# Optimization experiments

Measured on AMD Instinct MI355X. Metric: run time of the kernel, lower is better.

## Reference

```python
import jax, jax.numpy as jnp
import numpy as np

SEQ_LEN, BATCH, INPUT_SIZE, HIDDEN_SIZE = 512, 256, 256, 1024
ALPHA = 10.0 / 100.0  # dt / tau


def setup_inputs() -> dict:
    key = jax.random.key(0)
    k1, k2, k3, k4, k5 = jax.random.split(key, 5)
    s_in = 1.0 / np.sqrt(INPUT_SIZE)
    s_hh = 1.0 / np.sqrt(HIDDEN_SIZE)
    return {
        "x": jax.random.normal(k1, (SEQ_LEN, BATCH, INPUT_SIZE), jnp.float32),
        "W_in": jax.random.uniform(k2, (HIDDEN_SIZE, INPUT_SIZE), jnp.float32, -s_in, s_in),
        "b_in": jax.random.uniform(k3, (HIDDEN_SIZE,), jnp.float32, -s_in, s_in),
        "W_hh": jax.random.uniform(k4, (HIDDEN_SIZE, HIDDEN_SIZE), jnp.float32, -s_hh, s_hh),
        "b_hh": jax.random.uniform(k5, (HIDDEN_SIZE,), jnp.float32, -s_hh, s_hh),
    }


def reference(x, W_in, b_in, W_hh, b_hh):
    # Precompute input projection for all steps as one batched GEMM: [T,B,H]
    inp_proj = jnp.einsum("tbi,hi->tbh", x, W_in) + b_in

    def step(hidden, u_t):
        h_new = jax.nn.relu(u_t + hidden @ W_hh.T + b_hh)
        h_new = hidden * (1.0 - ALPHA) + h_new * ALPHA
        return h_new, h_new

    h0 = jnp.zeros((x.shape[1], W_hh.shape[0]), x.dtype)
    hidden, output = jax.lax.scan(step, h0, inp_proj)
    return output, hidden
```

## Files before the change

kernel.cpp:

```cpp
#include <hip/hip_runtime.h>
#include <hip/hip_bf16.h>
#include <stdint.h>
#include <stddef.h>

#define T_LEN 512
#define B_SZ  256
#define I_SZ  256
#define H_SZ  1024
#define NGRP  16

typedef __attribute__((ext_vector_type(8))) short bf16x8;
typedef __attribute__((ext_vector_type(4))) float f32x4;
typedef __attribute__((ext_vector_type(4))) unsigned int u32x4;
typedef unsigned short u16;
typedef unsigned int   u32;
typedef unsigned long long u64;

__device__ inline u16 f2bf(float f) {
  union { float f; u32 u; } x; x.f = f;
  u32 r = x.u + 0x7fffu + ((x.u >> 16) & 1u);
  return (u16)(r >> 16);
}

#define GLDS16(gp, lp) __builtin_amdgcn_global_load_lds( \
    (const __attribute__((address_space(1))) u32*)(gp),  \
    (__attribute__((address_space(3))) u32*)(lp), 16, 0, 0)

#define PIN8(B, i) asm volatile("" : "+v"(B[i]), "+v"(B[i+1]), "+v"(B[i+2]), \
    "+v"(B[i+3]), "+v"(B[i+4]), "+v"(B[i+5]), "+v"(B[i+6]), "+v"(B[i+7]))
#define PIN32(B) do { PIN8(B,0); PIN8(B,8); PIN8(B,16); PIN8(B,24); } while (0)

struct GCnt { u32 v; u32 pad[31]; };

__global__ __launch_bounds__(256) void cvt_kernel(const float* __restrict__ src,
                                                  u16* __restrict__ dst, int n) {
  int stride = gridDim.x * blockDim.x * 4;
  for (int i = (blockIdx.x * blockDim.x + threadIdx.x) * 4; i < n; i += stride) {
    float4 v = *reinterpret_cast<const float4*>(src + i);
    ushort4 o;
    o.x = f2bf(v.x); o.y = f2bf(v.y); o.z = f2bf(v.z); o.w = f2bf(v.w);
    *reinterpret_cast<ushort4*>(dst + i) = o;
  }
}

__global__ __launch_bounds__(256) void stage1_gemm(const u16* __restrict__ A,
                                                   const u16* __restrict__ Bw,
                                                   const float* __restrict__ b_in,
                                                   float* __restrict__ C) {
  __shared__ __align__(16) u16 As[128 * 32];
  __shared__ __align__(16) u16 Bs[128 * 32];
  const int tid  = threadIdx.x;
  const int lane = tid & 63;
  const int wid  = tid >> 6;
  const int wr   = wid >> 1, wc = wid & 1;
  const int bm0  = blockIdx.x * 128;
  const int bn0  = blockIdx.y * 128;
  const int rl   = lane & 15;
  const int kl   = (lane >> 4) * 8;

  f32x4 acc[4][4];
  for (int mi = 0; mi < 4; ++mi)
    for (int ni = 0; ni < 4; ++ni)
      acc[mi][ni] = (f32x4){0.f, 0.f, 0.f, 0.f};

  for (int kt = 0; kt < I_SZ / 32; ++kt) {
    const int k0 = kt * 32;
    __syncthreads();
    for (int t2 = 0; t2 < 2; ++t2) {
      int c = t2 * 256 + tid;
      int row = c >> 2, c8 = c & 3;
      GLDS16(A  + (size_t)(bm0 + row) * I_SZ + k0 + c8 * 8, As + c * 8);
      GLDS16(Bw + (size_t)(bn0 + row) * I_SZ + k0 + c8 * 8, Bs + c * 8);
    }
    __syncthreads();
    bf16x8 af[4], bfv[4];
    for (int mi = 0; mi < 4; ++mi)
      af[mi] = *reinterpret_cast<const bf16x8*>(&As[(wr * 64 + mi * 16 + rl) * 32 + kl]);
    for (int ni = 0; ni < 4; ++ni)
      bfv[ni] = *reinterpret_cast<const bf16x8*>(&Bs[(wc * 64 + ni * 16 + rl) * 32 + kl]);
    for (int mi = 0; mi < 4; ++mi)
      for (int ni = 0; ni < 4; ++ni)
        acc[mi][ni] = __builtin_amdgcn_mfma_f32_16x16x32_bf16(af[mi], bfv[ni], acc[mi][ni], 0, 0, 0);
  }

  const int rh = (lane >> 4) * 4;
  for (int ni = 0; ni < 4; ++ni) {
    int col = bn0 + wc * 64 + ni * 16 + rl;
    float bi = b_in[col];
    for (int mi = 0; mi < 4; ++mi) {
      int row = bm0 + wr * 64 + mi * 16 + rh;
      f32x4 c = acc[mi][ni];
      for (int r = 0; r < 4; ++r)
        C[(size_t)(row + r) * H_SZ + col] = c[r] + bi;
    }
  }
}

__global__ __launch_bounds__(256, 1) void rnn_persistent(
    const u16* __restrict__ Whh, const float* __restrict__ b_hh,
    float* __restrict__ out, u16* __restrict__ hb0, u16* __restrict__ hb1,
    GCnt* __restrict__ cnts) {
  __shared__ __align__(16) u16 As[16 * 1024];

  const int b   = blockIdx.x;
  const int mg  = ((b & 7) << 1) | ((b >> 3) & 1);
  const int ng  = b >> 4;
  const int bm0 = mg * 16;
  const int bn0 = ng * 64;
  const int tid = threadIdx.x, lane = tid & 63, wid = tid >> 6;
  const int rl  = lane & 15, kq = lane >> 4;

  u32* cnt = &cnts[mg].v;

  const int wcol = bn0 + wid * 16 + rl;
  bf16x8 Breg[32];
#pragma unroll
  for (int kc = 0; kc < 32; ++kc)
    Breg[kc] = *reinterpret_cast<const bf16x8*>(Whh + (size_t)wcol * H_SZ + kc * 32 + kq * 8);
  PIN32(Breg);

  const int row = bm0 + rl;
  const int c0  = bn0 + wid * 16 + kq * 4;
  const float4 bh4 = *reinterpret_cast<const float4*>(b_hh + c0);

  float4 hprev = {0.f, 0.f, 0.f, 0.f};
  float4 u = *reinterpret_cast<const float4*>(out + (size_t)row * H_SZ + c0);
  const char* Asb = (const char*)As;

  const int wb = (tid & 127) * 16;
  const int rb = tid >> 7;

  for (int t = 0; t < T_LEN; ++t) {
    const u16* hin = (t & 1) ? hb1 : hb0;
    u16* hout      = (t & 1) ? hb0 : hb1;

    PIN32(Breg);

    u32x4 sv[8];
    const char* hinb = (const char*)hin;
#pragma unroll
    for (int i = 0; i < 8; ++i) {
      int r_ = 2 * i + rb;
      const void* src = hinb + (size_t)(bm0 + r_) * 2048 + wb;
      asm volatile("global_load_dwordx4 %0, %1, off sc0 sc1"
                   : "=v"(sv[i]) : "v"(src) : "memory");
    }
    asm volatile("s_waitcnt vmcnt(0)" ::: "memory");
    __builtin_amdgcn_sched_barrier(0);
#pragma unroll
    for (int i = 0; i < 8; ++i) {
      int r_ = 2 * i + rb;
      int dst = r_ * 2048 + (wb ^ ((r_ & 7) << 4));
      *reinterpret_cast<u32x4*>((char*)As + dst) = sv[i];
    }
    __syncthreads();

    float4 un = *reinterpret_cast<const float4*>(
        out + (size_t)(t + 1) * (B_SZ * H_SZ) + (size_t)row * H_SZ + c0);

    PIN32(Breg);

    f32x4 acc0 = (f32x4){0.f, 0.f, 0.f, 0.f};
    f32x4 acc1 = (f32x4){0.f, 0.f, 0.f, 0.f};
#pragma unroll
    for (int kc = 0; kc < 32; kc += 2) {
      bf16x8 a0 = *reinterpret_cast<const bf16x8*>(
          Asb + rl * 2048 + ((kc * 64 + kq * 16) ^ ((rl & 7) << 4)));
      acc0 = __builtin_amdgcn_mfma_f32_16x16x32_bf16(Breg[kc], a0, acc0, 0, 0, 0);
      bf16x8 a1 = *reinterpret_cast<const bf16x8*>(
          Asb + rl * 2048 + (((kc + 1) * 64 + kq * 16) ^ ((rl & 7) << 4)));
      acc1 = __builtin_amdgcn_mfma_f32_16x16x32_bf16(Breg[kc + 1], a1, acc1, 0, 0, 0);
    }

    float hv[4];
#pragma unroll
    for (int r = 0; r < 4; ++r) {
      float pre = (&u.x)[r] + acc0[r] + acc1[r] + (&bh4.x)[r];
      float hn  = fmaxf(pre, 0.f);
      float h   = (&hprev.x)[r] * 0.9f + hn * 0.1f;
      (&hprev.x)[r] = h;
      hv[r] = h;
    }
    u32 lo = (u32)f2bf(hv[0]) | ((u32)f2bf(hv[1]) << 16);
    u32 hi = (u32)f2bf(hv[2]) | ((u32)f2bf(hv[3]) << 16);
    u64 pk = (u64)lo | ((u64)hi << 32);
    __hip_atomic_store(reinterpret_cast<u64*>(hout + (size_t)row * H_SZ + c0), pk,
                       __ATOMIC_RELAXED, __HIP_MEMORY_SCOPE_AGENT);

    __syncthreads();
    if (t < T_LEN - 1 && tid == 0)
      __hip_atomic_fetch_add(cnt, 1u, __ATOMIC_RELAXED, __HIP_MEMORY_SCOPE_AGENT);

    float4 ho = {hv[0], hv[1], hv[2], hv[3]};
    *reinterpret_cast<float4*>(out + (size_t)t * (B_SZ * H_SZ) +
                               (size_t)row * H_SZ + c0) = ho;
    if (t == T_LEN - 1)
      *reinterpret_cast<float4*>(out + (size_t)T_LEN * (B_SZ * H_SZ) +
                                 (size_t)row * H_SZ + c0) = ho;
    u = un;

    if (t < T_LEN - 1) {
      if (tid == 0) {
        const u32 tgt = (u32)(NGRP * (t + 1));
        while (__hip_atomic_load(cnt, __ATOMIC_RELAXED, __HIP_MEMORY_SCOPE_AGENT) < tgt) {
        }
      }
      __syncthreads();
      __builtin_amdgcn_sched_barrier(0);
    }
  }
}

extern "C" void kernel_launch(void* const* d_in, const int* in_sizes, int n_in,
                              void* d_out, int out_size, void* d_ws, size_t ws_size,
                              hipStream_t stream) {
  const float* x    = (const float*)d_in[0];
  const float* W_in = (const float*)d_in[1];
  const float* b_in = (const float*)d_in[2];
  const float* W_hh = (const float*)d_in[3];
  const float* b_hh = (const float*)d_in[4];
  float* out = (float*)d_out;

  const size_t off_xb  = 0;
  const size_t off_wib = 67108864;
  const size_t off_whb = 67633152;
  const size_t off_hb0 = 69730304;
  const size_t off_hb1 = 70254592;
  const size_t need    = 70778880;
  if (ws_size < need) return;

  char* ws = (char*)d_ws;
  u16* xb   = (u16*)(ws + off_xb);
  u16* wib  = (u16*)(ws + off_wib);
  u16* whb  = (u16*)(ws + off_whb);
  u16* hb0  = (u16*)(ws + off_hb0);
  u16* hb1  = (u16*)(ws + off_hb1);
  GCnt* cnts = (GCnt*)(ws + 0);

  cvt_kernel<<<1024, 256, 0, stream>>>(x,    xb,  T_LEN * B_SZ * I_SZ);
  cvt_kernel<<<64,   256, 0, stream>>>(W_in, wib, H_SZ * I_SZ);
  cvt_kernel<<<256,  256, 0, stream>>>(W_hh, whb, H_SZ * H_SZ);
  hipMemsetAsync(hb0, 0, (size_t)B_SZ * H_SZ * sizeof(u16), stream);

  dim3 g1(T_LEN * B_SZ / 128, H_SZ / 128);
  stage1_gemm<<<g1, 256, 0, stream>>>(xb, wib, b_in, out);

  hipMemsetAsync(cnts, 0, NGRP * sizeof(GCnt), stream);

  rnn_persistent<<<256, 256, 0, stream>>>(whb, b_hh, out, hb0, hb1, cnts);
}
```

Measured before the change: 1.342 ms.

## Fuse input projection into persistent RNN kernel, drop stage1 GEMM

Removes the separate x conversion kernel and the stage-1 GEMM. W_in is now held in registers inside the persistent recurrent kernel, which converts the x slice for the next step to bf16 in LDS (double buffered) while waiting on the barrier, then adds it through extra MFMAs each step. This drops a large GEMM plus its write and read of the projection tensor. In exchange each step does more compute and global loads on the serial critical path, and register pressure rises.

```diff
diff --git a/kernel.cpp b/kernel.cpp
--- a/kernel.cpp
+++ b/kernel.cpp
@@ -21,10 +21,6 @@
   u32 r = x.u + 0x7fffu + ((x.u >> 16) & 1u);
   return (u16)(r >> 16);
 }
-
-#define GLDS16(gp, lp) __builtin_amdgcn_global_load_lds( \
-    (const __attribute__((address_space(1))) u32*)(gp),  \
-    (__attribute__((address_space(3))) u32*)(lp), 16, 0, 0)
 
 #define PIN8(B, i) asm volatile("" : "+v"(B[i]), "+v"(B[i+1]), "+v"(B[i+2]), \
     "+v"(B[i+3]), "+v"(B[i+4]), "+v"(B[i+5]), "+v"(B[i+6]), "+v"(B[i+7]))
@@ -43,64 +39,13 @@
   }
 }
 
-__global__ __launch_bounds__(256) void stage1_gemm(const u16* __restrict__ A,
-                                                   const u16* __restrict__ Bw,
-                                                   const float* __restrict__ b_in,
-                                                   float* __restrict__ C) {
-  __shared__ __align__(16) u16 As[128 * 32];
-  __shared__ __align__(16) u16 Bs[128 * 32];
-  const int tid  = threadIdx.x;
-  const int lane = tid & 63;
-  const int wid  = tid >> 6;
-  const int wr   = wid >> 1, wc = wid & 1;
-  const int bm0  = blockIdx.x * 128;
-  const int bn0  = blockIdx.y * 128;
-  const int rl   = lane & 15;
-  const int kl   = (lane >> 4) * 8;
-
-  f32x4 acc[4][4];
-  for (int mi = 0; mi < 4; ++mi)
-    for (int ni = 0; ni < 4; ++ni)
-      acc[mi][ni] = (f32x4){0.f, 0.f, 0.f, 0.f};
-
-  for (int kt = 0; kt < I_SZ / 32; ++kt) {
-    const int k0 = kt * 32;
-    __syncthreads();
-    for (int t2 = 0; t2 < 2; ++t2) {
-      int c = t2 * 256 + tid;
-      int row = c >> 2, c8 = c & 3;
-      GLDS16(A  + (size_t)(bm0 + row) * I_SZ + k0 + c8 * 8, As + c * 8);
-      GLDS16(Bw + (size_t)(bn0 + row) * I_SZ + k0 + c8 * 8, Bs + c * 8);
-    }
-    __syncthreads();
-    bf16x8 af[4], bfv[4];
-    for (int mi = 0; mi < 4; ++mi)
-      af[mi] = *reinterpret_cast<const bf16x8*>(&As[(wr * 64 + mi * 16 + rl) * 32 + kl]);
-    for (int ni = 0; ni < 4; ++ni)
-      bfv[ni] = *reinterpret_cast<const bf16x8*>(&Bs[(wc * 64 + ni * 16 + rl) * 32 + kl]);
-    for (int mi = 0; mi < 4; ++mi)
-      for (int ni = 0; ni < 4; ++ni)
-        acc[mi][ni] = __builtin_amdgcn_mfma_f32_16x16x32_bf16(af[mi], bfv[ni], acc[mi][ni], 0, 0, 0);
-  }
-
-  const int rh = (lane >> 4) * 4;
-  for (int ni = 0; ni < 4; ++ni) {
-    int col = bn0 + wc * 64 + ni * 16 + rl;
-    float bi = b_in[col];
-    for (int mi = 0; mi < 4; ++mi) {
-      int row = bm0 + wr * 64 + mi * 16 + rh;
-      f32x4 c = acc[mi][ni];
-      for (int r = 0; r < 4; ++r)
-        C[(size_t)(row + r) * H_SZ + col] = c[r] + bi;
-    }
-  }
-}
-
 __global__ __launch_bounds__(256, 1) void rnn_persistent(
-    const u16* __restrict__ Whh, const float* __restrict__ b_hh,
-    float* __restrict__ out, u16* __restrict__ hb0, u16* __restrict__ hb1,
-    GCnt* __restrict__ cnts) {
+    const float* __restrict__ x, const u16* __restrict__ Win,
+    const u16* __restrict__ Whh, const float* __restrict__ b_in,
+    const float* __restrict__ b_hh, float* __restrict__ out,
+    u16* __restrict__ hb0, u16* __restrict__ hb1, GCnt* __restrict__ cnts) {
   __shared__ __align__(16) u16 As[16 * 1024];
+  __shared__ __align__(16) u16 Xs[2][16 * 256];
 
   const int b   = blockIdx.x;
   const int mg  = ((b & 7) << 1) | ((b >> 3) & 1);
@@ -117,18 +62,50 @@
 #pragma unroll
   for (int kc = 0; kc < 32; ++kc)
     Breg[kc] = *reinterpret_cast<const bf16x8*>(Whh + (size_t)wcol * H_SZ + kc * 32 + kq * 8);
+  bf16x8 Wreg[8];
+#pragma unroll
+  for (int kc = 0; kc < 8; ++kc)
+    Wreg[kc] = *reinterpret_cast<const bf16x8*>(Win + (size_t)wcol * I_SZ + kc * 32 + kq * 8);
   PIN32(Breg);
+  PIN8(Wreg, 0);
 
   const int row = bm0 + rl;
   const int c0  = bn0 + wid * 16 + kq * 4;
-  const float4 bh4 = *reinterpret_cast<const float4*>(b_hh + c0);
+  float4 bsum;
+#pragma unroll
+  for (int r = 0; r < 4; ++r)
+    (&bsum.x)[r] = b_in[c0 + r] + b_hh[c0 + r];
 
   float4 hprev = {0.f, 0.f, 0.f, 0.f};
-  float4 u = *reinterpret_cast<const float4*>(out + (size_t)row * H_SZ + c0);
   const char* Asb = (const char*)As;
 
   const int wb = (tid & 127) * 16;
   const int rb = tid >> 7;
+
+  const int xc0 = tid * 2;
+
+  auto stage_x = [&](int s) {
+    const float* xs = x + (size_t)s * (B_SZ * I_SZ);
+#pragma unroll
+    for (int j = 0; j < 2; ++j) {
+      int c  = xc0 + j;
+      int r_ = c >> 5;
+      int cb = (c & 31) * 16;
+      const float* src = xs + (size_t)(bm0 + r_) * I_SZ + (c & 31) * 8;
+      float4 f0 = *reinterpret_cast<const float4*>(src);
+      float4 f1 = *reinterpret_cast<const float4*>(src + 4);
+      u32x4 v;
+      v.x = (u32)f2bf(f0.x) | ((u32)f2bf(f0.y) << 16);
+      v.y = (u32)f2bf(f0.z) | ((u32)f2bf(f0.w) << 16);
+      v.z = (u32)f2bf(f1.x) | ((u32)f2bf(f1.y) << 16);
+      v.w = (u32)f2bf(f1.z) | ((u32)f2bf(f1.w) << 16);
+      int dst = r_ * 512 + (cb ^ ((r_ & 7) << 4));
+      *reinterpret_cast<u32x4*>((char*)Xs[s & 1] + dst) = v;
+    }
+  };
+
+  stage_x(0);
+  __syncthreads();
 
   for (int t = 0; t < T_LEN; ++t) {
     const u16* hin = (t & 1) ? hb1 : hb0;
@@ -155,13 +132,11 @@
     }
     __syncthreads();
 
-    float4 un = *reinterpret_cast<const float4*>(
-        out + (size_t)(t + 1) * (B_SZ * H_SZ) + (size_t)row * H_SZ + c0);
-
     PIN32(Breg);
 
     f32x4 acc0 = (f32x4){0.f, 0.f, 0.f, 0.f};
     f32x4 acc1 = (f32x4){0.f, 0.f, 0.f, 0.f};
+    f32x4 acc2 = (f32x4){0.f, 0.f, 0.f, 0.f};
 #pragma unroll
     for (int kc = 0; kc < 32; kc += 2) {
       bf16x8 a0 = *reinterpret_cast<const bf16x8*>(
@@ -171,11 +146,20 @@
           Asb + rl * 2048 + (((kc + 1) * 64 + kq * 16) ^ ((rl & 7) << 4)));
       acc1 = __builtin_amdgcn_mfma_f32_16x16x32_bf16(Breg[kc + 1], a1, acc1, 0, 0, 0);
     }
+    {
+      const char* Xb = (const char*)Xs[t & 1];
+#pragma unroll
+      for (int kc = 0; kc < 8; ++kc) {
+        bf16x8 xa = *reinterpret_cast<const bf16x8*>(
+            Xb + rl * 512 + ((kc * 64 + kq * 16) ^ ((rl & 7) << 4)));
+        acc2 = __builtin_amdgcn_mfma_f32_16x16x32_bf16(Wreg[kc], xa, acc2, 0, 0, 0);
+      }
+    }
 
     float hv[4];
 #pragma unroll
     for (int r = 0; r < 4; ++r) {
-      float pre = (&u.x)[r] + acc0[r] + acc1[r] + (&bh4.x)[r];
+      float pre = acc0[r] + acc1[r] + acc2[r] + (&bsum.x)[r];
       float hn  = fmaxf(pre, 0.f);
       float h   = (&hprev.x)[r] * 0.9f + hn * 0.1f;
       (&hprev.x)[r] = h;
@@ -191,13 +175,13 @@
     if (t < T_LEN - 1 && tid == 0)
       __hip_atomic_fetch_add(cnt, 1u, __ATOMIC_RELAXED, __HIP_MEMORY_SCOPE_AGENT);
 
+    if (t < T_LEN - 1) stage_x(t + 1);
     float4 ho = {hv[0], hv[1], hv[2], hv[3]};
     *reinterpret_cast<float4*>(out + (size_t)t * (B_SZ * H_SZ) +
                                (size_t)row * H_SZ + c0) = ho;
     if (t == T_LEN - 1)
       *reinterpret_cast<float4*>(out + (size_t)T_LEN * (B_SZ * H_SZ) +
                                  (size_t)row * H_SZ + c0) = ho;
-    u = un;
 
     if (t < T_LEN - 1) {
       if (tid == 0) {
@@ -221,31 +205,26 @@
   const float* b_hh = (const float*)d_in[4];
   float* out = (float*)d_out;
 
-  const size_t off_xb  = 0;
-  const size_t off_wib = 67108864;
-  const size_t off_whb = 67633152;
-  const size_t off_hb0 = 69730304;
-  const size_t off_hb1 = 70254592;
-  const size_t need    = 70778880;
+  const size_t off_wib = 0;
+  const size_t off_whb = 524288;
+  const size_t off_hb0 = 2621440;
+  const size_t off_hb1 = 3145728;
+  const size_t off_cnt = 3670016;
+  const size_t need    = 3672064;
   if (ws_size < need) return;
 
   char* ws = (char*)d_ws;
-  u16* xb   = (u16*)(ws + off_xb);
   u16* wib  = (u16*)(ws + off_wib);
   u16* whb  = (u16*)(ws + off_whb);
   u16* hb0  = (u16*)(ws + off_hb0);
   u16* hb1  = (u16*)(ws + off_hb1);
-  GCnt* cnts = (GCnt*)(ws + 0);
-
-  cvt_kernel<<<1024, 256, 0, stream>>>(x,    xb,  T_LEN * B_SZ * I_SZ);
-  cvt_kernel<<<64,   256, 0, stream>>>(W_in, wib, H_SZ * I_SZ);
-  cvt_kernel<<<256,  256, 0, stream>>>(W_hh, whb, H_SZ * H_SZ);
+  GCnt* cnts = (GCnt*)(ws + off_cnt);
+
+  cvt_kernel<<<64,  256, 0, stream>>>(W_in, wib, H_SZ * I_SZ);
+  cvt_kernel<<<256, 256, 0, stream>>>(W_hh, whb, H_SZ * H_SZ);
   hipMemsetAsync(hb0, 0, (size_t)B_SZ * H_SZ * sizeof(u16), stream);
-
-  dim3 g1(T_LEN * B_SZ / 128, H_SZ / 128);
-  stage1_gemm<<<g1, 256, 0, stream>>>(xb, wib, b_in, out);
-
   hipMemsetAsync(cnts, 0, NGRP * sizeof(GCnt), stream);
 
-  rnn_persistent<<<256, 256, 0, stream>>>(whb, b_hh, out, hb0, hb1, cnts);
-}
+  rnn_persistent<<<256, 256, 0, stream>>>(x, wib, whb, b_in, b_hh,
+                                          out, hb0, hb1, cnts);
+}
```

New measurement: 1.695 ms. +26.3%, slower.
